# Kernel tuning notes

Measured on AMD Instinct MI355X. Metric: run time of the kernel, lower is better.

Reference implementation:

```python
import jax, jax.numpy as jnp
import numpy as np

B, S, H = 2, 2048, 1024
NH = 16
HD = H // NH


def setup_inputs() -> dict:
    key = jax.random.key(0)
    ks = jax.random.split(key, 5)
    X = jax.random.normal(ks[0], (B, S, H), dtype=jnp.float32)
    mask = jnp.ones((B, S), dtype=jnp.int32)
    W_Q = jax.random.normal(ks[1], (H, H), dtype=jnp.float32) * 0.02
    W_K = jax.random.normal(ks[2], (H, H), dtype=jnp.float32) * 0.02
    W_V = jax.random.normal(ks[3], (H, H), dtype=jnp.float32) * 0.02
    W_O = jax.random.normal(ks[4], (H, H), dtype=jnp.float32) * 0.02
    return {"X": X, "mask": mask, "W_Q": W_Q, "W_K": W_K, "W_V": W_V, "W_O": W_O}


def reference(X, mask, W_Q, W_K, W_V, W_O):
    b, s, h = X.shape
    scaling = HD ** -0.5
    # project and split heads: [b, nh, s, hd]
    Q = (X @ W_Q).reshape(b, s, NH, HD).transpose(0, 2, 1, 3)
    K = (X @ W_K).reshape(b, s, NH, HD).transpose(0, 2, 1, 3)
    V = (X @ W_V).reshape(b, s, NH, HD).transpose(0, 2, 1, 3)
    scores = jnp.einsum('bhqd,bhkd->bhqk', Q, K) * scaling
    scores = jnp.clip(scores, -10000.0, 10000.0)
    # 2D mask [b, s] -> broadcast as [b, 1, 1, s]; fill -inf where mask == 0
    m = mask[:, None, None, :]
    scores = jnp.where(m == 0, -jnp.inf, scores)
    attn = jax.nn.softmax(scores, axis=-1)
    # dropout is identity in eval / p=0
    context = jnp.einsum('bhqk,bhkd->bhqd', attn, V)
    context = context.transpose(0, 2, 1, 3).reshape(b, s, h)
    return context @ W_O
```

## Files before the change

### kernel.cpp

```cpp
#include <hip/hip_runtime.h>
#include <hip/hip_bf16.h>

#define S_LEN 2048
#define HDIM  1024
#define NHEADS 16
#define HD    64
#define QKV_STRIDE (S_LEN * 2 * HDIM)

typedef __attribute__((ext_vector_type(8))) short short8;
typedef __attribute__((ext_vector_type(4))) float float4v;

__device__ __forceinline__ unsigned short f2bf(float f) {
  return (unsigned short)((__builtin_bit_cast(unsigned int, f) + 0x8000u) >> 16);
}
__device__ __forceinline__ unsigned int pkbf(float a, float b) {
  unsigned int ua = __builtin_bit_cast(unsigned int, a) + 0x8000u;
  unsigned int ub = __builtin_bit_cast(unsigned int, b) + 0x8000u;
  return __builtin_amdgcn_perm(ub, ua, 0x07060302u);
}

__device__ __forceinline__ void async_copy16(const void* g, void* l) {
  __builtin_amdgcn_global_load_lds((__attribute__((address_space(1))) const void*)g,
                                   (__attribute__((address_space(3))) void*)l, 16, 0, 0);
}

__global__ void prep_kernel(const float* __restrict__ X, unsigned short* __restrict__ Xb,
                            const float* __restrict__ W0, const float* __restrict__ W1,
                            const float* __restrict__ W2, const float* __restrict__ W3,
                            unsigned short* __restrict__ Wt) {
  __shared__ unsigned short tile[64][72];
  const int t = threadIdx.x;
  if (blockIdx.x < 4096) {
    int i = blockIdx.x * 256 + t;
    float4 v = ((const float4*)X)[i];
    uint2 o;
    o.x = pkbf(v.x, v.y);
    o.y = pkbf(v.z, v.w);
    ((uint2*)Xb)[i] = o;
    return;
  }
  const int wid = blockIdx.x - 4096;
  const int z = wid >> 8;
  const int rem = wid & 255;
  const int n0 = (rem & 15) * 64;
  const int k0 = (rem >> 4) * 64;
  const float* W = (z == 0) ? W0 : (z == 1) ? W1 : (z == 2) ? W2 : W3;
  unsigned short* out = Wt + (size_t)z * HDIM * HDIM;
#pragma unroll
  for (int it = 0; it < 4; ++it) {
    int idx = it * 256 + t;
    int r  = idx >> 4;
    int c4 = (idx & 15) * 4;
    float4 v = *(const float4*)&W[(size_t)(k0 + r) * HDIM + n0 + c4];
    tile[c4 + 0][r] = f2bf(v.x);
    tile[c4 + 1][r] = f2bf(v.y);
    tile[c4 + 2][r] = f2bf(v.z);
    tile[c4 + 3][r] = f2bf(v.w);
  }
  __syncthreads();
#pragma unroll
  for (int it = 0; it < 4; ++it) {
    int idx = it * 256 + t;
    int r  = idx >> 4;
    int c4 = (idx & 15) * 4;
    ushort4 o;
    o.x = tile[r][c4 + 0]; o.y = tile[r][c4 + 1];
    o.z = tile[r][c4 + 2]; o.w = tile[r][c4 + 3];
    *(ushort4*)&out[(size_t)(n0 + r) * HDIM + k0 + c4] = o;
  }
}

__global__ __launch_bounds__(256, 2) void gemm_qkv_kernel(
    const unsigned short* __restrict__ A,
    const unsigned short* __restrict__ Wt,
    unsigned short* __restrict__ out)
{
  __shared__ unsigned short sA[128 * 32];
  __shared__ unsigned short sB[3 * 64 * 32];
  const int m0 = blockIdx.x * 128;
  const int n0 = blockIdx.y * 64;
  const int t = threadIdx.x;
  const int lane = t & 63;
  const int w = t >> 6;
  const int wm = w & 1, wn = w >> 1;

  const int sr  = lane >> 2;
  const int scp = lane & 3;
  const int scl = scp ^ ((sr >> 1) & 3);
  const long ga0 = (long)(m0 + 16 * w + sr) * HDIM + scl * 8;
  const long ga1 = ga0 + 64l * HDIM;
  const long gb  = (long)(n0 + 16 * w + sr) * HDIM + scl * 8;
  unsigned short* lA0 = &sA[(16 * w) * 32];
  unsigned short* lA1 = &sA[(64 + 16 * w) * 32];
  unsigned short* lB  = &sB[(16 * w) * 32];

  const int fr = lane & 15;
  const int fq = lane >> 4;
  int offA[4], offB[2];
#pragma unroll
  for (int i = 0; i < 4; ++i) {
    int ra = wm * 64 + i * 16 + fr;
    offA[i] = ra * 32 + (fq ^ ((ra >> 1) & 3)) * 8;
  }
#pragma unroll
  for (int i = 0; i < 2; ++i) {
    int rb = wn * 32 + i * 16 + fr;
    offB[i] = rb * 32 + (fq ^ ((rb >> 1) & 3)) * 8;
  }

  float4v acc[3][4][2] = {};

  for (int kk = 0; kk < HDIM; kk += 32) {
    __syncthreads();
    async_copy16(A + ga0 + kk, lA0);
    async_copy16(A + ga1 + kk, lA1);
#pragma unroll
    for (int z = 0; z < 3; ++z)
      async_copy16(Wt + (long)z * (HDIM * HDIM) + gb + kk, lB + z * 2048);
    __syncthreads();
    short8 af[4];
#pragma unroll
    for (int i = 0; i < 4; ++i) af[i] = *(const short8*)&sA[offA[i]];
#pragma unroll
    for (int z = 0; z < 3; ++z) {
      short8 b0 = *(const short8*)&sB[z * 2048 + offB[0]];
      short8 b1 = *(const short8*)&sB[z * 2048 + offB[1]];
#pragma unroll
      for (int mi = 0; mi < 4; ++mi) {
        acc[z][mi][0] = __builtin_amdgcn_mfma_f32_16x16x32_bf16(af[mi], b0, acc[z][mi][0], 0, 0, 0);
        acc[z][mi][1] = __builtin_amdgcn_mfma_f32_16x16x32_bf16(af[mi], b1, acc[z][mi][1], 0, 0, 0);
      }
    }
  }

#pragma unroll
  for (int z = 0; z < 3; z += 2) {
    const float scle = (z == 0) ? 0.18033688011112042f : 1.0f;
    unsigned short* o = out + (size_t)z * QKV_STRIDE;
#pragma unroll
    for (int mi = 0; mi < 4; ++mi)
#pragma unroll
      for (int ni = 0; ni < 2; ++ni) {
        int m = m0 + wm * 64 + mi * 16 + fq * 4;
        int n = n0 + wn * 32 + ni * 16 + fr;
        int b = m >> 11, s = m & 2047, hh = n >> 6, d = n & 63;
        uint2 pk;
        pk.x = pkbf(acc[z][mi][ni][0] * scle, acc[z][mi][ni][1] * scle);
        pk.y = pkbf(acc[z][mi][ni][2] * scle, acc[z][mi][ni][3] * scle);
        *(uint2*)&o[(((size_t)(b * NHEADS + hh)) * HD + d) * S_LEN + s] = pk;
      }
  }
  {
    unsigned short* o = out + (size_t)QKV_STRIDE;
#pragma unroll
    for (int mi = 0; mi < 4; ++mi)
#pragma unroll
      for (int ni = 0; ni < 2; ++ni)
#pragma unroll
        for (int rg = 0; rg < 4; ++rg) {
          int m = m0 + wm * 64 + mi * 16 + fq * 4 + rg;
          int n = n0 + wn * 32 + ni * 16 + fr;
          int b = m >> 11, s = m & 2047, hh = n >> 6, d = n & 63;
          o[(((size_t)(b * NHEADS + hh)) * S_LEN + s) * HD + d] = f2bf(acc[1][mi][ni][rg]);
        }
  }
}

__global__ __launch_bounds__(256, 3) void gemm128_kernel(
    const unsigned short* __restrict__ A,
    const unsigned short* __restrict__ Bt,
    float* __restrict__ out)
{
  __shared__ unsigned short sA[128 * 32];
  __shared__ unsigned short sB[128 * 32];
  const int m0 = blockIdx.x * 128;
  const int n0 = blockIdx.y * 128;
  const int t = threadIdx.x;
  const int lane = t & 63;
  const int w = t >> 6;
  const int wm = w & 1, wn = w >> 1;

  const int sr  = lane >> 2;
  const int scp = lane & 3;
  const int scl = scp ^ ((sr >> 1) & 3);
  const long ga0 = (long)(m0 + 16 * w + sr) * HDIM + scl * 8;
  const long ga1 = ga0 + 64l * HDIM;
  const long gb0 = (long)(n0 + 16 * w + sr) * HDIM + scl * 8;
  const long gb1 = gb0 + 64l * HDIM;
  unsigned short* lA0 = &sA[(16 * w) * 32];
  unsigned short* lA1 = &sA[(64 + 16 * w) * 32];
  unsigned short* lB0 = &sB[(16 * w) * 32];
  unsigned short* lB1 = &sB[(64 + 16 * w) * 32];

  const int fr = lane & 15;
  const int fq = lane >> 4;
  int offA[4], offB[4];
#pragma unroll
  for (int i = 0; i < 4; ++i) {
    int ra = wm * 64 + i * 16 + fr;
    offA[i] = ra * 32 + (fq ^ ((ra >> 1) & 3)) * 8;
    int rb = wn * 64 + i * 16 + fr;
    offB[i] = rb * 32 + (fq ^ ((rb >> 1) & 3)) * 8;
  }

  float4v acc[4][4] = {};

  for (int kk = 0; kk < HDIM; kk += 32) {
    __syncthreads();
    async_copy16(A + ga0 + kk, lA0);
    async_copy16(A + ga1 + kk, lA1);
    async_copy16(Bt + gb0 + kk, lB0);
    async_copy16(Bt + gb1 + kk, lB1);
    __syncthreads();
    short8 af[4], bf[4];
#pragma unroll
    for (int i = 0; i < 4; ++i) af[i] = *(const short8*)&sA[offA[i]];
#pragma unroll
    for (int i = 0; i < 4; ++i) bf[i] = *(const short8*)&sB[offB[i]];
#pragma unroll
    for (int mi = 0; mi < 4; ++mi)
#pragma unroll
      for (int ni = 0; ni < 4; ++ni)
        acc[mi][ni] = __builtin_amdgcn_mfma_f32_16x16x32_bf16(af[mi], bf[ni], acc[mi][ni], 0, 0, 0);
  }

#pragma unroll
  for (int mi = 0; mi < 4; ++mi)
#pragma unroll
    for (int ni = 0; ni < 4; ++ni)
#pragma unroll
      for (int rg = 0; rg < 4; ++rg) {
        int m = m0 + wm * 64 + mi * 16 + fq * 4 + rg;
        int n = n0 + wn * 64 + ni * 16 + fr;
        out[(size_t)m * HDIM + n] = acc[mi][ni][rg];
      }
}

__device__ __forceinline__ void stage_tile(char* smem, const unsigned short* Kp,
    const unsigned short* Vtp, size_t base, int tile, int w, int kr, int kc) {
  const int kv = tile * 64;
  char* bufb = smem + (tile & 1) * 16384;
  unsigned short* dK = (unsigned short*)bufb + (w * 8) * 64;
  async_copy16(Kp + base + (size_t)(kv + w * 8 + kr) * HD + ((kc ^ kr) * 8), dK);
  unsigned short* dV = (unsigned short*)(bufb + 8192) + (w * 8) * 64;
  const int d = w * 8 + kr;
  async_copy16(Vtp + base + (size_t)d * S_LEN + kv + ((kc ^ kr) * 8), dV);
}

__global__ __launch_bounds__(512, 4) void attn_kernel(
    const unsigned short* __restrict__ Qtp,
    const unsigned short* __restrict__ Kp,
    const unsigned short* __restrict__ Vtp,
    const int* __restrict__ mask,
    unsigned short* __restrict__ ctx)
{
  __shared__ __align__(16) char smem[53248];

  const int bh = blockIdx.y;
  const int b = bh >> 4;
  const int h = bh & 15;
  const size_t base = (size_t)bh * (S_LEN * HD);
  const int q0 = blockIdx.x * 128;
  const int t = threadIdx.x;
  const int lane = t & 63;
  const int w = t >> 6;
  const int qg = w >> 1;
  const int kh = w & 1;
  const int fr = lane & 15;
  const int fq = lane >> 4;
  const int kr = lane >> 3, kc = lane & 7;
  unsigned short* sPw = (unsigned short*)(smem + 32768) + w * (32 * 40);

  short8 qfr[2][2];
#pragma unroll
  for (int q_ = 0; q_ < 2; ++q_)
#pragma unroll
    for (int ks = 0; ks < 2; ++ks)
#pragma unroll
      for (int j = 0; j < 8; ++j)
        qfr[q_][ks][j] = (short)Qtp[base + (size_t)(ks * 32 + fq * 8 + j) * S_LEN
                                    + (q0 + qg * 32 + q_ * 16 + fr)];

  float l_lane[2] = {0.f, 0.f};
  float4v o_acc[4][2] = {};
  const float4v zero4 = {0.f, 0.f, 0.f, 0.f};

  int mnext = mask[b * S_LEN + lane];

  stage_tile(smem, Kp, Vtp, base, 0, w, kr, kc);

#pragma unroll 2
  for (int it = 0; it < 32; ++it) {
    __syncthreads();
    if (it < 31)
      stage_tile(smem, Kp, Vtp, base, it + 1, w, kr, kc);

    unsigned long long bal = __ballot(mnext != 0);
    if (it < 31)
      mnext = mask[b * S_LEN + (it + 1) * 64 + lane];

    const unsigned short* sKb  = (const unsigned short*)(smem + (it & 1) * 16384);
    const unsigned short* sVtb = (const unsigned short*)(smem + (it & 1) * 16384 + 8192);

    float4v s_acc[2][2];
#pragma unroll
    for (int kf = 0; kf < 2; ++kf) {
      int rk = kh * 32 + kf * 16 + fr;
      short8 k0 = *(const short8*)&sKb[rk * 64 + ((fq ^ (rk & 7)) * 8)];
      short8 k1 = *(const short8*)&sKb[rk * 64 + (((4 + fq) ^ (rk & 7)) * 8)];
#pragma unroll
      for (int q_ = 0; q_ < 2; ++q_) {
        float4v s = __builtin_amdgcn_mfma_f32_16x16x32_bf16(k0, qfr[q_][0], zero4, 0, 0, 0);
        s_acc[kf][q_] = __builtin_amdgcn_mfma_f32_16x16x32_bf16(k1, qfr[q_][1], s, 0, 0, 0);
      }
    }

    short8 vf[4];
#pragma unroll
    for (int df = 0; df < 4; ++df) {
      int rv = df * 16 + fr;
      vf[df] = *(const short8*)&sVtb[rv * 64 + (((kh * 4 + fq) ^ (fr & 7)) * 8)];
    }

#pragma unroll
    for (int kf = 0; kf < 2; ++kf) {
      unsigned mseg = 0xFu;
      if (bal != ~0ull)
        mseg = (unsigned)(bal >> (kh * 32 + kf * 16 + fq * 4)) & 0xFu;
#pragma unroll
      for (int q_ = 0; q_ < 2; ++q_) {
        float p0 = __builtin_amdgcn_exp2f(s_acc[kf][q_][0]);
        float p1 = __builtin_amdgcn_exp2f(s_acc[kf][q_][1]);
        float p2 = __builtin_amdgcn_exp2f(s_acc[kf][q_][2]);
        float p3 = __builtin_amdgcn_exp2f(s_acc[kf][q_][3]);
        if (bal != ~0ull) {
          p0 = (mseg & 1u) ? p0 : 0.f;
          p1 = (mseg & 2u) ? p1 : 0.f;
          p2 = (mseg & 4u) ? p2 : 0.f;
          p3 = (mseg & 8u) ? p3 : 0.f;
        }
        l_lane[q_] += (p0 + p1) + (p2 + p3);
        uint2 pk;
        pk.x = pkbf(p0, p1);
        pk.y = pkbf(p2, p3);
        *(uint2*)&sPw[(q_ * 16 + fr) * 40 + (kf * 4 + fq) * 4] = pk;
      }
    }

    short8 pf[2];
#pragma unroll
    for (int q_ = 0; q_ < 2; ++q_)
      pf[q_] = *(const short8*)&sPw[(q_ * 16 + fr) * 40 + fq * 8];
#pragma unroll
    for (int df = 0; df < 4; ++df)
#pragma unroll
      for (int q_ = 0; q_ < 2; ++q_)
        o_acc[df][q_] = __builtin_amdgcn_mfma_f32_16x16x32_bf16(vf[df], pf[q_], o_acc[df][q_], 0, 0, 0);
  }

#pragma unroll
  for (int q_ = 0; q_ < 2; ++q_) {
    l_lane[q_] += __shfl_xor(l_lane[q_], 16);
    l_lane[q_] += __shfl_xor(l_lane[q_], 32);
  }

  __syncthreads();
  float* red = (float*)smem;
  float* rec = red + (size_t)(qg * 64 + lane) * 34;
  if (kh) {
#pragma unroll
    for (int df = 0; df < 4; ++df)
#pragma unroll
      for (int q_ = 0; q_ < 2; ++q_) {
        int e = df * 2 + q_;
        *(float2*)&rec[4 * e]     = make_float2(o_acc[df][q_][0], o_acc[df][q_][1]);
        *(float2*)&rec[4 * e + 2] = make_float2(o_acc[df][q_][2], o_acc[df][q_][3]);
      }
    *(float2*)&rec[32] = make_float2(l_lane[0], l_lane[1]);
  }
  __syncthreads();
  if (!kh) {
#pragma unroll
    for (int df = 0; df < 4; ++df)
#pragma unroll
      for (int q_ = 0; q_ < 2; ++q_) {
        int e = df * 2 + q_;
        float2 a = *(float2*)&rec[4 * e];
        float2 c = *(float2*)&rec[4 * e + 2];
        o_acc[df][q_][0] += a.x; o_acc[df][q_][1] += a.y;
        o_acc[df][q_][2] += c.x; o_acc[df][q_][3] += c.y;
      }
    float2 lr = *(float2*)&rec[32];
    float inv_l[2];
    inv_l[0] = 1.0f / (l_lane[0] + lr.x);
    inv_l[1] = 1.0f / (l_lane[1] + lr.y);
#pragma unroll
    for (int q_ = 0; q_ < 2; ++q_) {
      size_t rowoff = ((size_t)(b * S_LEN + q0 + qg * 32 + q_ * 16 + fr)) * HDIM + h * HD;
#pragma unroll
      for (int df = 0; df < 4; ++df) {
        uint2 pk;
        pk.x = pkbf(o_acc[df][q_][0] * inv_l[q_], o_acc[df][q_][1] * inv_l[q_]);
        pk.y = pkbf(o_acc[df][q_][2] * inv_l[q_], o_acc[df][q_][3] * inv_l[q_]);
        *(uint2*)&ctx[rowoff + df * 16 + fq * 4] = pk;
      }
    }
  }
}

extern "C" void kernel_launch(void* const* d_in, const int* in_sizes, int n_in,
                              void* d_out, int out_size, void* d_ws, size_t ws_size,
                              hipStream_t stream) {
  const float* X  = (const float*)d_in[0];
  const int* mask = (const int*)d_in[1];
  const float* Wq = (const float*)d_in[2];
  const float* Wk = (const float*)d_in[3];
  const float* Wv = (const float*)d_in[4];
  const float* Wo = (const float*)d_in[5];
  float* out = (float*)d_out;

  char* ws = (char*)d_ws;
  unsigned short* Xb  = (unsigned short*)(ws);
  unsigned short* Wt  = (unsigned short*)(ws + (8u << 20));
  unsigned short* QKV = (unsigned short*)(ws + (16u << 20));
  unsigned short* CTX = (unsigned short*)(ws);

  prep_kernel<<<5120, 256, 0, stream>>>(X, Xb, Wq, Wk, Wv, Wo, Wt);
  gemm_qkv_kernel<<<dim3(32, 16), 256, 0, stream>>>(Xb, Wt, QKV);
  attn_kernel<<<dim3(16, 32), 512, 0, stream>>>(
      QKV, QKV + QKV_STRIDE, QKV + 2 * (size_t)QKV_STRIDE, mask, CTX);
  gemm128_kernel<<<dim3(32, 8), 256, 0, stream>>>(CTX, Wt + (3u << 20), out);
}
```

Before: 187.6 us.

## Double-buffer LDS tiles in QKV and output projection GEMMs

Both the fused QKV GEMM and the 128x128 output GEMM now keep two LDS buffers per operand. The async global-to-LDS copy for the next K step is issued right after the barrier, so it can overlap the MFMA work on the current step, and one of the two barriers per iteration is dropped. The cost is double the shared memory per block and a dependence on the compiler not inserting conservative vmcnt waits before the LDS reads, which would serialize the copies again.

```diff
diff --git a/kernel.cpp b/kernel.cpp
--- a/kernel.cpp
+++ b/kernel.cpp
@@ -75,8 +75,8 @@
     const unsigned short* __restrict__ Wt,
     unsigned short* __restrict__ out)
 {
-  __shared__ unsigned short sA[128 * 32];
-  __shared__ unsigned short sB[3 * 64 * 32];
+  __shared__ unsigned short sA[2 * 128 * 32];
+  __shared__ unsigned short sB[2 * 3 * 64 * 32];
   const int m0 = blockIdx.x * 128;
   const int n0 = blockIdx.y * 64;
   const int t = threadIdx.x;
@@ -90,9 +90,6 @@
   const long ga0 = (long)(m0 + 16 * w + sr) * HDIM + scl * 8;
   const long ga1 = ga0 + 64l * HDIM;
   const long gb  = (long)(n0 + 16 * w + sr) * HDIM + scl * 8;
-  unsigned short* lA0 = &sA[(16 * w) * 32];
-  unsigned short* lA1 = &sA[(64 + 16 * w) * 32];
-  unsigned short* lB  = &sB[(16 * w) * 32];
 
   const int fr = lane & 15;
   const int fq = lane >> 4;
@@ -110,21 +107,31 @@
 
   float4v acc[3][4][2] = {};
 
-  for (int kk = 0; kk < HDIM; kk += 32) {
+  auto stage = [&](int ks) {
+    const int kk = ks * 32;
+    unsigned short* A0 = &sA[(ks & 1) * 4096 + (16 * w) * 32];
+    unsigned short* Bb = &sB[(ks & 1) * 6144 + (16 * w) * 32];
+    async_copy16(A + ga0 + kk, A0);
+    async_copy16(A + ga1 + kk, A0 + 2048);
+#pragma unroll
+    for (int z = 0; z < 3; ++z)
+      async_copy16(Wt + (long)z * (HDIM * HDIM) + gb + kk, Bb + z * 2048);
+  };
+
+  stage(0);
+#pragma unroll 2
+  for (int ks = 0; ks < 32; ++ks) {
     __syncthreads();
-    async_copy16(A + ga0 + kk, lA0);
-    async_copy16(A + ga1 + kk, lA1);
-#pragma unroll
-    for (int z = 0; z < 3; ++z)
-      async_copy16(Wt + (long)z * (HDIM * HDIM) + gb + kk, lB + z * 2048);
-    __syncthreads();
+    if (ks < 31) stage(ks + 1);
+    const unsigned short* a  = &sA[(ks & 1) * 4096];
+    const unsigned short* bb = &sB[(ks & 1) * 6144];
     short8 af[4];
 #pragma unroll
-    for (int i = 0; i < 4; ++i) af[i] = *(const short8*)&sA[offA[i]];
+    for (int i = 0; i < 4; ++i) af[i] = *(const short8*)&a[offA[i]];
 #pragma unroll
     for (int z = 0; z < 3; ++z) {
-      short8 b0 = *(const short8*)&sB[z * 2048 + offB[0]];
-      short8 b1 = *(const short8*)&sB[z * 2048 + offB[1]];
+      short8 b0 = *(const short8*)&bb[z * 2048 + offB[0]];
+      short8 b1 = *(const short8*)&bb[z * 2048 + offB[1]];
 #pragma unroll
       for (int mi = 0; mi < 4; ++mi) {
         acc[z][mi][0] = __builtin_amdgcn_mfma_f32_16x16x32_bf16(af[mi], b0, acc[z][mi][0], 0, 0, 0);
@@ -171,8 +178,8 @@
     const unsigned short* __restrict__ Bt,
     float* __restrict__ out)
 {
-  __shared__ unsigned short sA[128 * 32];
-  __shared__ unsigned short sB[128 * 32];
+  __shared__ unsigned short sA[2 * 128 * 32];
+  __shared__ unsigned short sB[2 * 128 * 32];
   const int m0 = blockIdx.x * 128;
   const int n0 = blockIdx.y * 128;
   const int t = threadIdx.x;
@@ -187,10 +194,6 @@
   const long ga1 = ga0 + 64l * HDIM;
   const long gb0 = (long)(n0 + 16 * w + sr) * HDIM + scl * 8;
   const long gb1 = gb0 + 64l * HDIM;
-  unsigned short* lA0 = &sA[(16 * w) * 32];
-  unsigned short* lA1 = &sA[(64 + 16 * w) * 32];
-  unsigned short* lB0 = &sB[(16 * w) * 32];
-  unsigned short* lB1 = &sB[(64 + 16 * w) * 32];
 
   const int fr = lane & 15;
   const int fq = lane >> 4;
@@ -205,18 +208,28 @@
 
   float4v acc[4][4] = {};
 
-  for (int kk = 0; kk < HDIM; kk += 32) {
+  auto stage = [&](int ks) {
+    const int kk = ks * 32;
+    unsigned short* A0 = &sA[(ks & 1) * 4096 + (16 * w) * 32];
+    unsigned short* B0 = &sB[(ks & 1) * 4096 + (16 * w) * 32];
+    async_copy16(A + ga0 + kk, A0);
+    async_copy16(A + ga1 + kk, A0 + 2048);
+    async_copy16(Bt + gb0 + kk, B0);
+    async_copy16(Bt + gb1 + kk, B0 + 2048);
+  };
+
+  stage(0);
+#pragma unroll 2
+  for (int ks = 0; ks < 32; ++ks) {
     __syncthreads();
-    async_copy16(A + ga0 + kk, lA0);
-    async_copy16(A + ga1 + kk, lA1);
-    async_copy16(Bt + gb0 + kk, lB0);
-    async_copy16(Bt + gb1 + kk, lB1);
-    __syncthreads();
+    if (ks < 31) stage(ks + 1);
+    const unsigned short* a = &sA[(ks & 1) * 4096];
+    const unsigned short* bp = &sB[(ks & 1) * 4096];
     short8 af[4], bf[4];
 #pragma unroll
-    for (int i = 0; i < 4; ++i) af[i] = *(const short8*)&sA[offA[i]];
-#pragma unroll
-    for (int i = 0; i < 4; ++i) bf[i] = *(const short8*)&sB[offB[i]];
+    for (int i = 0; i < 4; ++i) af[i] = *(const short8*)&a[offA[i]];
+#pragma unroll
+    for (int i = 0; i < 4; ++i) bf[i] = *(const short8*)&bp[offB[i]];
 #pragma unroll
     for (int mi = 0; mi < 4; ++mi)
 #pragma unroll
```

Result: no change. 188.1 us (+0.3%).
